# Optimization experiments

Hardware: AMD Instinct MI355X
Metric: run time of the kernel (lower is better)

Reference implementation:

```python
import jax, jax.numpy as jnp
import numpy as np

STATE_DIM = 64
HIDDEN_DIM = 256
BATCH = 4096
DT = 0.01


def setup_inputs() -> dict:
    key = jax.random.key(0)
    ks = jax.random.split(key, 7)
    s = 1.0 / np.sqrt(STATE_DIM)
    h = 1.0 / np.sqrt(HIDDEN_DIM)
    return {
        "x0": jax.random.normal(ks[0], (BATCH, STATE_DIM), dtype=jnp.float32),
        "W1": jax.random.uniform(ks[1], (STATE_DIM, HIDDEN_DIM), jnp.float32, -s, s),
        "b1": jax.random.uniform(ks[2], (HIDDEN_DIM,), jnp.float32, -s, s),
        "W2": jax.random.uniform(ks[3], (HIDDEN_DIM, HIDDEN_DIM), jnp.float32, -h, h),
        "b2": jax.random.uniform(ks[4], (HIDDEN_DIM,), jnp.float32, -h, h),
        "W3": jax.random.uniform(ks[5], (HIDDEN_DIM, STATE_DIM), jnp.float32, -h, h),
        "b3": jax.random.uniform(ks[6], (STATE_DIM,), jnp.float32, -h, h),
        "dt_scale": jnp.ones((1,), dtype=jnp.float32) * 0.01,
        "steps": 200,
    }


def reference(x0, W1, b1, W2, b2, W3, b3, dt_scale, steps):
    def func(x):
        h1 = jnp.tanh(x @ W1 + b1)
        h2 = jnp.tanh(h1 @ W2 + b2)
        return h2 @ W3 + b3

    def step(x, _):
        x_next = x + func(x) * dt_scale * DT  # Euler update
        return x_next, x_next

    _, traj = jax.lax.scan(step, x0, None, length=steps)
    # traj: [steps, batch, state_dim] -> [batch, steps+1, state_dim]
    return jnp.concatenate([x0[:, None, :], jnp.swapaxes(traj, 0, 1)], axis=1)
```

## Files before the change

kernel.cpp:

```cpp
#include <hip/hip_runtime.h>


#define STATE_DIM 64
#define HIDDEN    256
#define TILE_M    16
#define NBLK      256
#define XPITCH    68
#define HPITCH    260
#define LOG2E2    2.8853900817779268f

typedef short v8s __attribute__((ext_vector_type(8)));
typedef float v4f __attribute__((ext_vector_type(4)));

__device__ __forceinline__ unsigned short f2bf(float f) {
    return (unsigned short)((__float_as_uint(f) + 0x8000u) >> 16);
}
__device__ __forceinline__ unsigned pk2bf(float a, float b) {
#if __has_builtin(__builtin_amdgcn_perm)
    return __builtin_amdgcn_perm(__float_as_uint(b) + 0x8000u,
                                 __float_as_uint(a) + 0x8000u,
                                 0x07060302u);
#else
    return ((__float_as_uint(a) + 0x8000u) >> 16) |
           ((__float_as_uint(b) + 0x8000u) & 0xffff0000u);
#endif
}
__device__ __forceinline__ float fast_tanh_pre(float a) {
    float e = __builtin_amdgcn_exp2f(a);
    return fmaf(-2.0f, __builtin_amdgcn_rcpf(e + 1.0f), 1.0f);
}
__device__ __forceinline__ void sync_lds() {
    asm volatile("s_waitcnt lgkmcnt(0)" ::: "memory");
    __builtin_amdgcn_s_barrier();
    asm volatile("" ::: "memory");
}

__global__ void prep_weights(const float* __restrict__ W1,
                             const float* __restrict__ W2,
                             const float* __restrict__ W3,
                             short* __restrict__ W1t,
                             short* __restrict__ W2t,
                             short* __restrict__ W3t) {
    int u = blockIdx.x * 256 + threadIdx.x;
    if (u < 65536) {
        int n = u >> 8, k = u & 255;
        W2t[u] = (short)f2bf(W2[k * 256 + n] * LOG2E2);
    }
    int v = u - 65536;
    if (v >= 0 && v < 16384) {
        int n = v >> 6, k = v & 63;
        W1t[v] = (short)f2bf(W1[k * 256 + n] * LOG2E2);
    }
    int t = u - (65536 + 16384);
    if (t >= 0 && t < 16384) {
        int n = t >> 8, k = t & 255;
        W3t[t] = (short)f2bf(W3[k * 64 + n]);
    }
}

__global__ __launch_bounds__(512, 2)
void ode_kernel(const float* __restrict__ x0,
                const float* __restrict__ b1,
                const float* __restrict__ b2,
                const float* __restrict__ b3,
                const float* __restrict__ dt_scale,
                const int*   __restrict__ stepsp,
                const short* __restrict__ W1t,
                const short* __restrict__ W2t,
                const short* __restrict__ W3t,
                float* __restrict__ out) {
    __shared__ short xb [TILE_M * XPITCH];
    __shared__ short h1b[TILE_M * HPITCH];
    __shared__ short h2b[TILE_M * HPITCH];

    const int tid  = threadIdx.x;
    const int w    = tid >> 6;
    const int lane = tid & 63;
    const int ln   = lane & 15;
    const int q    = lane >> 4;
    const int blk  = blockIdx.x;
    const int nsteps = *stepsp;
    const float scale = dt_scale[0] * 0.01f;
    const int n0 = 32 * w;

    v8s w1f[2][2], w2f[2][8], w3f[8];
    #pragma unroll
    for (int t = 0; t < 2; t++)
        #pragma unroll
        for (int ks = 0; ks < 2; ks++)
            w1f[t][ks] = *(const v8s*)(W1t + (n0 + 16 * t + ln) * 64 + 32 * ks + 8 * q);
    #pragma unroll
    for (int t = 0; t < 2; t++)
        #pragma unroll
        for (int ks = 0; ks < 8; ks++)
            w2f[t][ks] = *(const v8s*)(W2t + (n0 + 16 * t + ln) * 256 + 32 * ks + 8 * q);
    if (w < 4) {
        #pragma unroll
        for (int ks = 0; ks < 8; ks++)
            w3f[ks] = *(const v8s*)(W3t + (16 * w + ln) * 256 + 32 * ks + 8 * q);
    }
    v4f b1v[2], b2v[2], b3v = {0.f, 0.f, 0.f, 0.f};
    #pragma unroll
    for (int t = 0; t < 2; t++) {
        b1v[t] = *(const v4f*)(b1 + n0 + 16 * t + 4 * q) * LOG2E2;
        b2v[t] = *(const v4f*)(b2 + n0 + 16 * t + 4 * q) * LOG2E2;
    }
    if (w < 4) b3v = *(const v4f*)(b3 + 16 * w + 4 * q);

    v4f x = {0.f, 0.f, 0.f, 0.f};
    unsigned tbase = 0;
    const int xw0 = ln * XPITCH + 16 * w + 4 * q;
    if (w < 4) {
        x = *(const v4f*)(x0 + (size_t)(blk * TILE_M + ln) * STATE_DIM + 16 * w + 4 * q);
        uint2 p; p.x = pk2bf(x[0], x[1]); p.y = pk2bf(x[2], x[3]);
        *(uint2*)(xb + xw0) = p;
        tbase = (unsigned)(blk * TILE_M + ln) * (unsigned)((nsteps + 1) * STATE_DIM)
              + 16 * w + 4 * q;
        *(v4f*)(out + tbase) = x;
        tbase += STATE_DIM;
    }
    __syncthreads();

    int xrd[2], hrd[8];
    #pragma unroll
    for (int ks = 0; ks < 2; ks++) xrd[ks] = ln * XPITCH + 32 * ks + 8 * q;
    #pragma unroll
    for (int ks = 0; ks < 8; ks++) hrd[ks] = ln * HPITCH + 32 * ks + 8 * q;
    const int hw0 = ln * HPITCH + n0 + 4 * q;

    for (int s = 0; s < nsteps; s++) {
        v8s xa0 = *(const v8s*)(xb + xrd[0]);
        v8s xa1 = *(const v8s*)(xb + xrd[1]);
        v4f a0 = b1v[0], a1 = b1v[1];
        a0 = __builtin_amdgcn_mfma_f32_16x16x32_bf16(w1f[0][0], xa0, a0, 0, 0, 0);
        a1 = __builtin_amdgcn_mfma_f32_16x16x32_bf16(w1f[1][0], xa0, a1, 0, 0, 0);
        a0 = __builtin_amdgcn_mfma_f32_16x16x32_bf16(w1f[0][1], xa1, a0, 0, 0, 0);
        a1 = __builtin_amdgcn_mfma_f32_16x16x32_bf16(w1f[1][1], xa1, a1, 0, 0, 0);
        {
            uint2 p0, p1;
            p0.x = pk2bf(fast_tanh_pre(a0[0]), fast_tanh_pre(a0[1]));
            p0.y = pk2bf(fast_tanh_pre(a0[2]), fast_tanh_pre(a0[3]));
            p1.x = pk2bf(fast_tanh_pre(a1[0]), fast_tanh_pre(a1[1]));
            p1.y = pk2bf(fast_tanh_pre(a1[2]), fast_tanh_pre(a1[3]));
            *(uint2*)(h1b + hw0)      = p0;
            *(uint2*)(h1b + hw0 + 16) = p1;
        }
        sync_lds();

        v8s ha[8];
        #pragma unroll
        for (int ks = 0; ks < 8; ks++) ha[ks] = *(const v8s*)(h1b + hrd[ks]);
        a0 = b2v[0]; a1 = b2v[1];
        #pragma unroll
        for (int ks = 0; ks < 8; ks++) {
            a0 = __builtin_amdgcn_mfma_f32_16x16x32_bf16(w2f[0][ks], ha[ks], a0, 0, 0, 0);
            a1 = __builtin_amdgcn_mfma_f32_16x16x32_bf16(w2f[1][ks], ha[ks], a1, 0, 0, 0);
        }
        {
            uint2 p0, p1;
            p0.x = pk2bf(fast_tanh_pre(a0[0]), fast_tanh_pre(a0[1]));
            p0.y = pk2bf(fast_tanh_pre(a0[2]), fast_tanh_pre(a0[3]));
            p1.x = pk2bf(fast_tanh_pre(a1[0]), fast_tanh_pre(a1[1]));
            p1.y = pk2bf(fast_tanh_pre(a1[2]), fast_tanh_pre(a1[3]));
            *(uint2*)(h2b + hw0)      = p0;
            *(uint2*)(h2b + hw0 + 16) = p1;
        }
        sync_lds();

        if (w < 4) {
            v8s hc[8];
            #pragma unroll
            for (int ks = 0; ks < 8; ks++) hc[ks] = *(const v8s*)(h2b + hrd[ks]);
            v4f a3 = b3v;
            #pragma unroll
            for (int ks = 0; ks < 8; ks++)
                a3 = __builtin_amdgcn_mfma_f32_16x16x32_bf16(w3f[ks], hc[ks], a3, 0, 0, 0);
            #pragma unroll
            for (int i = 0; i < 4; i++)
                x[i] = fmaf(a3[i], scale, x[i]);
            uint2 p; p.x = pk2bf(x[0], x[1]); p.y = pk2bf(x[2], x[3]);
            *(uint2*)(xb + xw0) = p;
            *(v4f*)(out + tbase) = x;
            tbase += STATE_DIM;
        }
        sync_lds();
    }
}

extern "C" void kernel_launch(void* const* d_in, const int* in_sizes, int n_in,
                              void* d_out, int out_size, void* d_ws, size_t ws_size,
                              hipStream_t stream) {
    const float* x0 = (const float*)d_in[0];
    const float* W1 = (const float*)d_in[1];
    const float* b1 = (const float*)d_in[2];
    const float* W2 = (const float*)d_in[3];
    const float* b2 = (const float*)d_in[4];
    const float* W3 = (const float*)d_in[5];
    const float* b3 = (const float*)d_in[6];
    const float* dt = (const float*)d_in[7];
    const int* steps = (const int*)d_in[8];

    short* W1t = (short*)d_ws;
    short* W2t = W1t + 64 * 256;
    short* W3t = W2t + 256 * 256;

    prep_weights<<<384, 256, 0, stream>>>(W1, W2, W3, W1t, W2t, W3t);
    ode_kernel<<<NBLK, 512, 0, stream>>>(x0, b1, b2, b3, dt, steps,
                                         W1t, W2t, W3t, (float*)d_out);
}
```

Before: 416.7 us.

## Quantize layer-2/3 weights and hidden activations to FP8 with scaled MFMA

Converts W2 and W3 to FP8 (pre-scaled by 64) and stores the tanh hidden activations as FP8 (scaled by 16), then uses the MI355 scaled 16x16x128 f8f6f4 MFMA with E8M0 scale factors to undo the scaling. This cuts the per-step MFMA count for layers 2 and 3 and shrinks LDS traffic and weight register footprint. It lowers numerical precision of the recurrent 200-step integration, which risks accuracy drift against the fp32 reference.

```diff
diff --git a/kernel.cpp b/kernel.cpp
--- a/kernel.cpp
+++ b/kernel.cpp
@@ -6,14 +6,21 @@
 #define TILE_M    16
 #define NBLK      256
 #define XPITCH    68
-#define HPITCH    260
+#define HQPITCH   272
 #define LOG2E2    2.8853900817779268f
+#define SCALE_A   0x79797979
+#define SCALE_B   0x7B7B7B7B
 
 typedef short v8s __attribute__((ext_vector_type(8)));
+typedef int   v8i __attribute__((ext_vector_type(8)));
 typedef float v4f __attribute__((ext_vector_type(4)));
 
 __device__ __forceinline__ unsigned short f2bf(float f) {
     return (unsigned short)((__float_as_uint(f) + 0x8000u) >> 16);
+}
+__device__ __forceinline__ unsigned char f2fp8(float f) {
+    int r = __builtin_amdgcn_cvt_pk_fp8_f32(f, 0.f, 0, false);
+    return (unsigned char)(r & 0xff);
 }
 __device__ __forceinline__ unsigned pk2bf(float a, float b) {
 #if __has_builtin(__builtin_amdgcn_perm)
@@ -25,9 +32,9 @@
            ((__float_as_uint(b) + 0x8000u) & 0xffff0000u);
 #endif
 }
-__device__ __forceinline__ float fast_tanh_pre(float a) {
+__device__ __forceinline__ float fast_tanh16(float a) {
     float e = __builtin_amdgcn_exp2f(a);
-    return fmaf(-2.0f, __builtin_amdgcn_rcpf(e + 1.0f), 1.0f);
+    return fmaf(-32.0f, __builtin_amdgcn_rcpf(e + 1.0f), 16.0f);
 }
 __device__ __forceinline__ void sync_lds() {
     asm volatile("s_waitcnt lgkmcnt(0)" ::: "memory");
@@ -39,12 +46,12 @@
                              const float* __restrict__ W2,
                              const float* __restrict__ W3,
                              short* __restrict__ W1t,
-                             short* __restrict__ W2t,
-                             short* __restrict__ W3t) {
+                             unsigned char* __restrict__ W2q,
+                             unsigned char* __restrict__ W3q) {
     int u = blockIdx.x * 256 + threadIdx.x;
     if (u < 65536) {
         int n = u >> 8, k = u & 255;
-        W2t[u] = (short)f2bf(W2[k * 256 + n] * LOG2E2);
+        W2q[u] = f2fp8(W2[k * 256 + n] * (LOG2E2 * 64.0f));
     }
     int v = u - 65536;
     if (v >= 0 && v < 16384) {
@@ -54,7 +61,7 @@
     int t = u - (65536 + 16384);
     if (t >= 0 && t < 16384) {
         int n = t >> 8, k = t & 255;
-        W3t[t] = (short)f2bf(W3[k * 64 + n]);
+        W3q[t] = f2fp8(W3[k * 64 + n] * 64.0f);
     }
 }
 
@@ -66,12 +73,12 @@
                 const float* __restrict__ dt_scale,
                 const int*   __restrict__ stepsp,
                 const short* __restrict__ W1t,
-                const short* __restrict__ W2t,
-                const short* __restrict__ W3t,
+                const unsigned char* __restrict__ W2q,
+                const unsigned char* __restrict__ W3q,
                 float* __restrict__ out) {
     __shared__ short xb [TILE_M * XPITCH];
-    __shared__ short h1b[TILE_M * HPITCH];
-    __shared__ short h2b[TILE_M * HPITCH];
+    __shared__ __attribute__((aligned(16))) unsigned char h1b[TILE_M * HQPITCH];
+    __shared__ __attribute__((aligned(16))) unsigned char h2b[TILE_M * HQPITCH];
 
     const int tid  = threadIdx.x;
     const int w    = tid >> 6;
@@ -83,7 +90,8 @@
     const float scale = dt_scale[0] * 0.01f;
     const int n0 = 32 * w;
 
-    v8s w1f[2][2], w2f[2][8], w3f[8];
+    v8s w1f[2][2];
+    v8i w2f[2][2], w3f[2];
     #pragma unroll
     for (int t = 0; t < 2; t++)
         #pragma unroll
@@ -92,12 +100,12 @@
     #pragma unroll
     for (int t = 0; t < 2; t++)
         #pragma unroll
-        for (int ks = 0; ks < 8; ks++)
-            w2f[t][ks] = *(const v8s*)(W2t + (n0 + 16 * t + ln) * 256 + 32 * ks + 8 * q);
+        for (int kk = 0; kk < 2; kk++)
+            w2f[t][kk] = *(const v8i*)(W2q + (n0 + 16 * t + ln) * 256 + 128 * kk + 32 * q);
     if (w < 4) {
         #pragma unroll
-        for (int ks = 0; ks < 8; ks++)
-            w3f[ks] = *(const v8s*)(W3t + (16 * w + ln) * 256 + 32 * ks + 8 * q);
+        for (int kk = 0; kk < 2; kk++)
+            w3f[kk] = *(const v8i*)(W3q + (16 * w + ln) * 256 + 128 * kk + 32 * q);
     }
     v4f b1v[2], b2v[2], b3v = {0.f, 0.f, 0.f, 0.f};
     #pragma unroll
@@ -121,12 +129,11 @@
     }
     __syncthreads();
 
-    int xrd[2], hrd[8];
+    int xrd[2];
     #pragma unroll
     for (int ks = 0; ks < 2; ks++) xrd[ks] = ln * XPITCH + 32 * ks + 8 * q;
-    #pragma unroll
-    for (int ks = 0; ks < 8; ks++) hrd[ks] = ln * HPITCH + 32 * ks + 8 * q;
-    const int hw0 = ln * HPITCH + n0 + 4 * q;
+    const int hq0 = ln * HQPITCH + 32 * q;
+    const int hwq = ln * HQPITCH + n0 + 4 * q;
 
     for (int s = 0; s < nsteps; s++) {
         v8s xa0 = *(const v8s*)(xb + xrd[0]);
@@ -137,44 +144,38 @@
         a0 = __builtin_amdgcn_mfma_f32_16x16x32_bf16(w1f[0][1], xa1, a0, 0, 0, 0);
         a1 = __builtin_amdgcn_mfma_f32_16x16x32_bf16(w1f[1][1], xa1, a1, 0, 0, 0);
         {
-            uint2 p0, p1;
-            p0.x = pk2bf(fast_tanh_pre(a0[0]), fast_tanh_pre(a0[1]));
-            p0.y = pk2bf(fast_tanh_pre(a0[2]), fast_tanh_pre(a0[3]));
-            p1.x = pk2bf(fast_tanh_pre(a1[0]), fast_tanh_pre(a1[1]));
-            p1.y = pk2bf(fast_tanh_pre(a1[2]), fast_tanh_pre(a1[3]));
-            *(uint2*)(h1b + hw0)      = p0;
-            *(uint2*)(h1b + hw0 + 16) = p1;
+            int p0 = __builtin_amdgcn_cvt_pk_fp8_f32(fast_tanh16(a0[0]), fast_tanh16(a0[1]), 0, false);
+            p0     = __builtin_amdgcn_cvt_pk_fp8_f32(fast_tanh16(a0[2]), fast_tanh16(a0[3]), p0, true);
+            int p1 = __builtin_amdgcn_cvt_pk_fp8_f32(fast_tanh16(a1[0]), fast_tanh16(a1[1]), 0, false);
+            p1     = __builtin_amdgcn_cvt_pk_fp8_f32(fast_tanh16(a1[2]), fast_tanh16(a1[3]), p1, true);
+            *(int*)(h1b + hwq)      = p0;
+            *(int*)(h1b + hwq + 16) = p1;
         }
         sync_lds();
 
-        v8s ha[8];
-        #pragma unroll
-        for (int ks = 0; ks < 8; ks++) ha[ks] = *(const v8s*)(h1b + hrd[ks]);
+        v8i hb0 = *(const v8i*)(h1b + hq0);
+        v8i hb1 = *(const v8i*)(h1b + hq0 + 128);
         a0 = b2v[0]; a1 = b2v[1];
-        #pragma unroll
-        for (int ks = 0; ks < 8; ks++) {
-            a0 = __builtin_amdgcn_mfma_f32_16x16x32_bf16(w2f[0][ks], ha[ks], a0, 0, 0, 0);
-            a1 = __builtin_amdgcn_mfma_f32_16x16x32_bf16(w2f[1][ks], ha[ks], a1, 0, 0, 0);
-        }
+        a0 = __builtin_amdgcn_mfma_scale_f32_16x16x128_f8f6f4(w2f[0][0], hb0, a0, 0, 0, 0, SCALE_A, 0, SCALE_B);
+        a1 = __builtin_amdgcn_mfma_scale_f32_16x16x128_f8f6f4(w2f[1][0], hb0, a1, 0, 0, 0, SCALE_A, 0, SCALE_B);
+        a0 = __builtin_amdgcn_mfma_scale_f32_16x16x128_f8f6f4(w2f[0][1], hb1, a0, 0, 0, 0, SCALE_A, 0, SCALE_B);
+        a1 = __builtin_amdgcn_mfma_scale_f32_16x16x128_f8f6f4(w2f[1][1], hb1, a1, 0, 0, 0, SCALE_A, 0, SCALE_B);
         {
-            uint2 p0, p1;
-            p0.x = pk2bf(fast_tanh_pre(a0[0]), fast_tanh_pre(a0[1]));
-            p0.y = pk2bf(fast_tanh_pre(a0[2]), fast_tanh_pre(a0[3]));
-            p1.x = pk2bf(fast_tanh_pre(a1[0]), fast_tanh_pre(a1[1]));
-            p1.y = pk2bf(fast_tanh_pre(a1[2]), fast_tanh_pre(a1[3]));
-            *(uint2*)(h2b + hw0)      = p0;
-            *(uint2*)(h2b + hw0 + 16) = p1;
+            int p0 = __builtin_amdgcn_cvt_pk_fp8_f32(fast_tanh16(a0[0]), fast_tanh16(a0[1]), 0, false);
+            p0     = __builtin_amdgcn_cvt_pk_fp8_f32(fast_tanh16(a0[2]), fast_tanh16(a0[3]), p0, true);
+            int p1 = __builtin_amdgcn_cvt_pk_fp8_f32(fast_tanh16(a1[0]), fast_tanh16(a1[1]), 0, false);
+            p1     = __builtin_amdgcn_cvt_pk_fp8_f32(fast_tanh16(a1[2]), fast_tanh16(a1[3]), p1, true);
+            *(int*)(h2b + hwq)      = p0;
+            *(int*)(h2b + hwq + 16) = p1;
         }
         sync_lds();
 
         if (w < 4) {
-            v8s hc[8];
-            #pragma unroll
-            for (int ks = 0; ks < 8; ks++) hc[ks] = *(const v8s*)(h2b + hrd[ks]);
+            v8i hc0 = *(const v8i*)(h2b + hq0);
+            v8i hc1 = *(const v8i*)(h2b + hq0 + 128);
             v4f a3 = b3v;
-            #pragma unroll
-            for (int ks = 0; ks < 8; ks++)
-                a3 = __builtin_amdgcn_mfma_f32_16x16x32_bf16(w3f[ks], hc[ks], a3, 0, 0, 0);
+            a3 = __builtin_amdgcn_mfma_scale_f32_16x16x128_f8f6f4(w3f[0], hc0, a3, 0, 0, 0, SCALE_A, 0, SCALE_B);
+            a3 = __builtin_amdgcn_mfma_scale_f32_16x16x128_f8f6f4(w3f[1], hc1, a3, 0, 0, 0, SCALE_A, 0, SCALE_B);
             #pragma unroll
             for (int i = 0; i < 4; i++)
                 x[i] = fmaf(a3[i], scale, x[i]);
@@ -201,10 +202,10 @@
     const int* steps = (const int*)d_in[8];
 
     short* W1t = (short*)d_ws;
-    short* W2t = W1t + 64 * 256;
-    short* W3t = W2t + 256 * 256;
-
-    prep_weights<<<384, 256, 0, stream>>>(W1, W2, W3, W1t, W2t, W3t);
+    unsigned char* W2q = (unsigned char*)(W1t + 16384);
+    unsigned char* W3q = W2q + 65536;
+
+    prep_weights<<<384, 256, 0, stream>>>(W1, W2, W3, W1t, W2q, W3q);
     ode_kernel<<<NBLK, 512, 0, stream>>>(x0, b1, b2, b3, dt, steps,
-                                         W1t, W2t, W3t, (float*)d_out);
-}
+                                         W1t, W2q, W3q, (float*)d_out);
+}
```

Measured after the change: 363.2 us. 1.15x faster.
